# Performance work log

Hardware: AMD Instinct MI355X
Metric: run time of the kernel (lower is better)

## Reference

```python
import jax, jax.numpy as jnp
import numpy as np

B, NQ, NK, D, DV = 16, 2048, 2048, 128, 128


def setup_inputs() -> dict:
    key = jax.random.key(0)
    kq, kk, kv, kl = jax.random.split(key, 4)
    return {
        "queries": jax.random.normal(kq, (B, NQ, D), dtype=jnp.float32),
        "keys": jax.random.normal(kk, (B, NK, D), dtype=jnp.float32),
        "values": jax.random.normal(kv, (B, NK, DV), dtype=jnp.float32),
        "valid_lens": jax.random.randint(kl, (B,), 1, NK + 1, dtype=jnp.int32),
    }


def reference(queries, keys, values, valid_lens):
    d = queries.shape[-1]
    # scores: [B, NQ, NK]
    scores = jnp.einsum("bqd,bkd->bqk", queries, keys) / jnp.sqrt(jnp.float32(d))
    # mask positions >= valid_len with -1e6 (matches sequence_mask semantics)
    key_pos = jnp.arange(scores.shape[-1], dtype=jnp.int32)  # [NK]
    mask = key_pos[None, None, :] < valid_lens[:, None, None]  # [B,1,NK] -> broadcast over queries
    scores = jnp.where(mask, scores, jnp.float32(-1000000.0))
    attn = jax.nn.softmax(scores, axis=-1)
    # dropout p=0.0 -> identity
    return jnp.einsum("bqk,bkv->bqv", attn, values)
```

## Files before the change

### kernel.cpp

```cpp
#include <hip/hip_runtime.h>


#define B_   16
#define NQ_  2048
#define NK_  2048
#define D_   128
#define DV_  128
#define NTASK_ 512

typedef unsigned short ushort;
typedef __attribute__((ext_vector_type(4))) float          f32x4;
typedef __attribute__((ext_vector_type(8))) __bf16         bf16x8;
typedef __attribute__((ext_vector_type(8))) unsigned short ushort8v;
typedef __attribute__((ext_vector_type(4))) unsigned int   uint4v;

#ifdef __has_builtin
#if __has_builtin(__builtin_amdgcn_cvt_pk_bf16_f32)
#define HAVE_CVT_PK_BF16 1
#endif
#endif

__device__ __forceinline__ ushort f2bf(float f) {
    unsigned u = __builtin_bit_cast(unsigned, f);
    return (ushort)((u + 0x8000u) >> 16);
}
__device__ __forceinline__ float bf2f(ushort h) {
    unsigned u = ((unsigned)h) << 16;
    return __builtin_bit_cast(float, u);
}
__device__ __forceinline__ unsigned f2bf2(float a, float b) {
#ifdef HAVE_CVT_PK_BF16
    auto t = __builtin_amdgcn_cvt_pk_bf16_f32(a, b);
    return __builtin_bit_cast(unsigned, t);
#else
    return (unsigned)f2bf(a) | ((unsigned)f2bf(b) << 16);
#endif
}

__device__ __forceinline__ void gl_lds16(const ushort* g, ushort* l) {
    __builtin_amdgcn_global_load_lds(
        (const __attribute__((address_space(1))) void*)g,
        (__attribute__((address_space(3))) void*)l, 16, 0, 0);
}

__global__ void make_schedule(const int* __restrict__ vlen, int* __restrict__ task) {
    __shared__ int s[16];
    int tid = threadIdx.x;
    if (tid < 16) {
        int my = vlen[tid];
        int rank = 0;
        for (int o = 0; o < 16; ++o) {
            int vo = vlen[o];
            if (vo > my || (vo == my && o < tid)) ++rank;
        }
        s[rank] = tid;
    }
    __syncthreads();
    for (int e = tid; e < NTASK_; e += 64) {
        int half = e >> 8;
        int r    = e & 255;
        int p    = r >> 5;
        int qt   = r & 31;
        int b    = half ? s[15 - p] : s[p];
        task[e]  = b | (qt << 8);
    }
}

__global__ __launch_bounds__(256) void convert_kv(
    const float* __restrict__ K, const float* __restrict__ V,
    const int* __restrict__ vlen, ushort* __restrict__ Kb, ushort* __restrict__ Vtb)
{
    const int id = blockIdx.x;
    const int b  = id & 15, kt = id >> 4;
    if (kt >= ((vlen[b] + 63) >> 6)) return;
    const int tid = threadIdx.x;
    const float* gK = K + ((size_t)b * NK_ + kt * 64) * D_;
    const float* gV = V + ((size_t)b * NK_ + kt * 64) * DV_;
    ushort* tK = Kb  + ((size_t)b * 32 + kt) * 8192;
    ushort* tV = Vtb + ((size_t)b * 32 + kt) * 8192;

    #pragma unroll
    for (int i = 0; i < 4; ++i) {
        int u = i * 256 + tid;
        int key = u >> 4, d8 = u & 15;
        const float* p = gK + key * D_ + d8 * 8;
        f32x4 a0 = *(const f32x4*)p;
        f32x4 a1 = *(const f32x4*)(p + 4);
        uint4v w;
        w[0] = f2bf2(a0[0], a0[1]); w[1] = f2bf2(a0[2], a0[3]);
        w[2] = f2bf2(a1[0], a1[1]); w[3] = f2bf2(a1[2], a1[3]);
        *(uint4v*)&tK[key * 128 + ((d8 ^ (key & 7)) << 3)] = w;
    }
    #pragma unroll
    for (int i = 0; i < 4; ++i) {
        int u = i * 256 + tid;
        int dv = u & 127, kg = u >> 7;
        const float* vp = gV + (size_t)(kg * 8) * DV_ + dv;
        float v[8];
        #pragma unroll
        for (int j = 0; j < 8; ++j) v[j] = vp[(size_t)j * DV_];
        uint4v w;
        w[0] = f2bf2(v[0], v[1]); w[1] = f2bf2(v[2], v[3]);
        w[2] = f2bf2(v[4], v[5]); w[3] = f2bf2(v[6], v[7]);
        *(uint4v*)&tV[dv * 64 + ((kg ^ (dv & 7)) << 3)] = w;
    }
}

__global__ __launch_bounds__(256, 2) void attn_fwd(
    const float* __restrict__ Q, const int* __restrict__ vlen,
    const int* __restrict__ task, const ushort* __restrict__ Kb,
    const ushort* __restrict__ Vtb, float* __restrict__ Out)
{
    __shared__ ushort KVbuf[2][16384];
    __shared__ ushort Pb[4][32][40];
    __shared__ float  lsh[2][64];
    float* Osh = (float*)&KVbuf[0][0];

    const int tid  = threadIdx.x;
    const int w    = tid >> 6;
    const int wq   = w >> 1;
    const int wk   = w & 1;
    const int L    = tid & 63;
    const int col  = L & 15;
    const int quad = L >> 4;

    const int tk    = task[blockIdx.x];
    const int b     = tk & 255;
    const int qbase = (tk >> 8) * 64;
    const int vl    = vlen[b];
    const int ntiles = (vl + 63) >> 6;

    const float qscale = 0.12751743f;
    bf16x8 qf[2][4];
    #pragma unroll
    for (int q16 = 0; q16 < 2; ++q16) {
        const int qrow = qbase + wq * 32 + q16 * 16 + col;
        const float* gQ = Q + ((size_t)b * NQ_ + qrow) * D_;
        #pragma unroll
        for (int c = 0; c < 4; ++c) {
            const float* p = gQ + c * 32 + quad * 8;
            f32x4 a0 = *(const f32x4*)p;
            f32x4 a1 = *(const f32x4*)(p + 4);
            uint4v us;
            us[0] = f2bf2(a0[0] * qscale, a0[1] * qscale);
            us[1] = f2bf2(a0[2] * qscale, a0[3] * qscale);
            us[2] = f2bf2(a1[0] * qscale, a1[1] * qscale);
            us[3] = f2bf2(a1[2] * qscale, a1[3] * qscale);
            qf[q16][c] = __builtin_bit_cast(bf16x8, us);
        }
    }

    f32x4 o[2][8];
    #pragma unroll
    for (int q16 = 0; q16 < 2; ++q16)
        #pragma unroll
        for (int d = 0; d < 8; ++d) o[q16][d] = (f32x4){0.f, 0.f, 0.f, 0.f};
    float l_run[2][4] = {{0.f,0.f,0.f,0.f},{0.f,0.f,0.f,0.f}};

    const ushort* tKb = Kb  + (size_t)b * 32 * 8192;
    const ushort* tVb = Vtb + (size_t)b * 32 * 8192;

    #define ISSUE_DMA(KT, BUF)                                               \
        do {                                                                 \
            const ushort* gk = tKb + (size_t)(KT) * 8192;                    \
            const ushort* gv = tVb + (size_t)(KT) * 8192;                    \
            _Pragma("unroll")                                                \
            for (int i = 0; i < 4; ++i) {                                    \
                int off = (i * 256 + tid) * 8;                               \
                gl_lds16(gk + off, &KVbuf[BUF][off]);                        \
                gl_lds16(gv + off, &KVbuf[BUF][8192 + off]);                 \
            }                                                                \
        } while (0)

    ISSUE_DMA(0, 0);

    for (int kt = 0; kt < ntiles; ++kt) {
        const int buf = kt & 1;
        __syncthreads();
        if (kt + 1 < ntiles) ISSUE_DMA(kt + 1, buf ^ 1);

        const ushort* Kt = &KVbuf[buf][0];
        const ushort* Vt = &KVbuf[buf][8192];
        const int k0 = kt * 64;

        f32x4 s[2][2];
        #pragma unroll
        for (int kc = 0; kc < 2; ++kc) {
            const int key = wk * 32 + kc * 16 + col;
            bf16x8 kb[4];
            #pragma unroll
            for (int c = 0; c < 4; ++c)
                kb[c] = __builtin_bit_cast(bf16x8, *(const ushort8v*)
                    &Kt[key * 128 + (((c * 4 + quad) ^ (col & 7)) << 3)]);
            #pragma unroll
            for (int q16 = 0; q16 < 2; ++q16) {
                f32x4 acc = (f32x4){0.f, 0.f, 0.f, 0.f};
                #pragma unroll
                for (int c = 0; c < 4; ++c)
                    acc = __builtin_amdgcn_mfma_f32_16x16x32_bf16(qf[q16][c], kb[c], acc, 0, 0, 0);
                s[q16][kc] = acc;
            }
        }

        if (k0 + 64 > vl) {
            #pragma unroll
            for (int kc = 0; kc < 2; ++kc)
                if (k0 + wk * 32 + kc * 16 + col >= vl) {
                    s[0][kc] = (f32x4){-1e30f,-1e30f,-1e30f,-1e30f};
                    s[1][kc] = (f32x4){-1e30f,-1e30f,-1e30f,-1e30f};
                }
        }

        #pragma unroll
        for (int q16 = 0; q16 < 2; ++q16)
            #pragma unroll
            for (int kc = 0; kc < 2; ++kc)
                #pragma unroll
                for (int r = 0; r < 4; ++r) {
                    ushort pb = f2bf(exp2f(s[q16][kc][r]));
                    Pb[w][q16 * 16 + quad * 4 + r][kc * 16 + col] = pb;
                    l_run[q16][r] += bf2f(pb);
                }


        bf16x8 pa[2];
        #pragma unroll
        for (int q16 = 0; q16 < 2; ++q16)
            pa[q16] = __builtin_bit_cast(bf16x8,
                *(const ushort8v*)&Pb[w][q16 * 16 + col][quad * 8]);
        #pragma unroll
        for (int dvc = 0; dvc < 8; ++dvc) {
            const int dv = dvc * 16 + col;
            bf16x8 vb = __builtin_bit_cast(bf16x8, *(const ushort8v*)
                &Vt[dv * 64 + (((wk * 4 + quad) ^ (col & 7)) << 3)]);
            #pragma unroll
            for (int q16 = 0; q16 < 2; ++q16)
                o[q16][dvc] = __builtin_amdgcn_mfma_f32_16x16x32_bf16(pa[q16], vb, o[q16][dvc], 0, 0, 0);
        }
    }
    #undef ISSUE_DMA

    #pragma unroll
    for (int off = 1; off < 16; off <<= 1)
        #pragma unroll
        for (int q16 = 0; q16 < 2; ++q16)
            #pragma unroll
            for (int r = 0; r < 4; ++r)
                l_run[q16][r] += __shfl_xor(l_run[q16][r], off, 64);

    __syncthreads();

    if (col == 0) {
        #pragma unroll
        for (int q16 = 0; q16 < 2; ++q16)
            #pragma unroll
            for (int r = 0; r < 4; ++r)
                lsh[wk][wq * 32 + q16 * 16 + quad * 4 + r] = l_run[q16][r];
    }
    #pragma unroll
    for (int q16 = 0; q16 < 2; ++q16)
        #pragma unroll
        for (int dvc = 0; dvc < 8; ++dvc)
            #pragma unroll
            for (int r = 0; r < 4; ++r)
                Osh[wk * 8192 + (wq * 32 + q16 * 16 + quad * 4 + r) * 128 + dvc * 16 + col]
                    = o[q16][dvc][r];
    __syncthreads();

    float* gO = Out + ((size_t)b * NQ_ + qbase) * DV_;
    #pragma unroll
    for (int i = 0; i < 8; ++i) {
        int idx = i * 256 + tid;
        int row = idx >> 5;
        int dq  = idx & 31;
        f32x4 a0 = *(const f32x4*)&Osh[row * 128 + dq * 4];
        f32x4 a1 = *(const f32x4*)&Osh[8192 + row * 128 + dq * 4];
        float linv = 1.0f / (lsh[0][row] + lsh[1][row]);
        f32x4 r = (a0 + a1) * linv;
        *(f32x4*)&gO[(size_t)row * DV_ + dq * 4] = r;
    }
}

extern "C" void kernel_launch(void* const* d_in, const int* in_sizes, int n_in,
                              void* d_out, int out_size, void* d_ws, size_t ws_size,
                              hipStream_t stream) {
    const float* Q  = (const float*)d_in[0];
    const float* K  = (const float*)d_in[1];
    const float* V  = (const float*)d_in[2];
    const int*   vl = (const int*)d_in[3];
    float* out = (float*)d_out;

    char* ws = (char*)d_ws;
    int* task = (int*)ws;
    ushort* Kbuf = (ushort*)(ws + 4096);
    ushort* Vbuf = Kbuf + (size_t)B_ * 32 * 8192;

    make_schedule<<<1, 64, 0, stream>>>(vl, task);
    convert_kv<<<dim3(512, 1, 1), dim3(256, 1, 1), 0, stream>>>(K, V, vl, Kbuf, Vbuf);
    attn_fwd<<<dim3(NTASK_, 1, 1), dim3(256, 1, 1), 0, stream>>>(
        Q, vl, task, Kbuf, Vbuf, out);
}
```

Before: 138.7 us.

## Restructure attention to 8 waves per block with register P transpose

The attention kernel now uses 512 threads per block, each wave handling 16 query rows instead of 32. The score MFMA is computed transposed so that P can be rearranged in registers with permlane swaps instead of going through LDS. The scheduling kernel is folded into the attention kernel, removing one launch. The change also adds s_setprio around the MFMA sections and a cheaper row-sum reduction. This trades more waves per block and less LDS traffic for redundant per-block ranking work and a different register and occupancy profile.

```diff
diff --git a/kernel.cpp b/kernel.cpp
--- a/kernel.cpp
+++ b/kernel.cpp
@@ -23,10 +23,6 @@
 __device__ __forceinline__ ushort f2bf(float f) {
     unsigned u = __builtin_bit_cast(unsigned, f);
     return (ushort)((u + 0x8000u) >> 16);
-}
-__device__ __forceinline__ float bf2f(ushort h) {
-    unsigned u = ((unsigned)h) << 16;
-    return __builtin_bit_cast(float, u);
 }
 __device__ __forceinline__ unsigned f2bf2(float a, float b) {
 #ifdef HAVE_CVT_PK_BF16
@@ -36,34 +32,15 @@
     return (unsigned)f2bf(a) | ((unsigned)f2bf(b) << 16);
 #endif
 }
-
+__device__ __forceinline__ float bfpair_sum(unsigned u) {
+    float lo = __builtin_bit_cast(float, u << 16);
+    float hi = __builtin_bit_cast(float, u & 0xffff0000u);
+    return lo + hi;
+}
 __device__ __forceinline__ void gl_lds16(const ushort* g, ushort* l) {
     __builtin_amdgcn_global_load_lds(
         (const __attribute__((address_space(1))) void*)g,
         (__attribute__((address_space(3))) void*)l, 16, 0, 0);
-}
-
-__global__ void make_schedule(const int* __restrict__ vlen, int* __restrict__ task) {
-    __shared__ int s[16];
-    int tid = threadIdx.x;
-    if (tid < 16) {
-        int my = vlen[tid];
-        int rank = 0;
-        for (int o = 0; o < 16; ++o) {
-            int vo = vlen[o];
-            if (vo > my || (vo == my && o < tid)) ++rank;
-        }
-        s[rank] = tid;
-    }
-    __syncthreads();
-    for (int e = tid; e < NTASK_; e += 64) {
-        int half = e >> 8;
-        int r    = e & 255;
-        int p    = r >> 5;
-        int qt   = r & 31;
-        int b    = half ? s[15 - p] : s[p];
-        task[e]  = b | (qt << 8);
-    }
 }
 
 __global__ __launch_bounds__(256) void convert_kv(
@@ -106,14 +83,14 @@
     }
 }
 
-__global__ __launch_bounds__(256, 2) void attn_fwd(
+__global__ __launch_bounds__(512, 4) void attn_fwd(
     const float* __restrict__ Q, const int* __restrict__ vlen,
-    const int* __restrict__ task, const ushort* __restrict__ Kb,
-    const ushort* __restrict__ Vtb, float* __restrict__ Out)
+    const ushort* __restrict__ Kb, const ushort* __restrict__ Vtb,
+    float* __restrict__ Out)
 {
     __shared__ ushort KVbuf[2][16384];
-    __shared__ ushort Pb[4][32][40];
     __shared__ float  lsh[2][64];
+    __shared__ int    ssch[16];
     float* Osh = (float*)&KVbuf[0][0];
 
     const int tid  = threadIdx.x;
@@ -124,38 +101,47 @@
     const int col  = L & 15;
     const int quad = L >> 4;
 
-    const int tk    = task[blockIdx.x];
-    const int b     = tk & 255;
-    const int qbase = (tk >> 8) * 64;
+    if (tid < 16) {
+        int my = vlen[tid];
+        int rank = 0;
+        for (int o = 0; o < 16; ++o) {
+            int vo = vlen[o];
+            if (vo > my || (vo == my && o < tid)) ++rank;
+        }
+        ssch[rank] = tid;
+    }
+    __syncthreads();
+
+    const int e     = blockIdx.x;
+    const int p_    = (e & 255) >> 5;
+    const int b     = (e >> 8) ? ssch[15 - p_] : ssch[p_];
+    const int qbase = (e & 31) * 64;
     const int vl    = vlen[b];
     const int ntiles = (vl + 63) >> 6;
 
     const float qscale = 0.12751743f;
-    bf16x8 qf[2][4];
-    #pragma unroll
-    for (int q16 = 0; q16 < 2; ++q16) {
-        const int qrow = qbase + wq * 32 + q16 * 16 + col;
+    bf16x8 qf[4];
+    {
+        const int qrow = qbase + wq * 16 + col;
         const float* gQ = Q + ((size_t)b * NQ_ + qrow) * D_;
         #pragma unroll
         for (int c = 0; c < 4; ++c) {
-            const float* p = gQ + c * 32 + quad * 8;
-            f32x4 a0 = *(const f32x4*)p;
-            f32x4 a1 = *(const f32x4*)(p + 4);
+            const float* pp = gQ + c * 32 + quad * 8;
+            f32x4 a0 = *(const f32x4*)pp;
+            f32x4 a1 = *(const f32x4*)(pp + 4);
             uint4v us;
             us[0] = f2bf2(a0[0] * qscale, a0[1] * qscale);
             us[1] = f2bf2(a0[2] * qscale, a0[3] * qscale);
             us[2] = f2bf2(a1[0] * qscale, a1[1] * qscale);
             us[3] = f2bf2(a1[2] * qscale, a1[3] * qscale);
-            qf[q16][c] = __builtin_bit_cast(bf16x8, us);
-        }
-    }
-
-    f32x4 o[2][8];
-    #pragma unroll
-    for (int q16 = 0; q16 < 2; ++q16)
-        #pragma unroll
-        for (int d = 0; d < 8; ++d) o[q16][d] = (f32x4){0.f, 0.f, 0.f, 0.f};
-    float l_run[2][4] = {{0.f,0.f,0.f,0.f},{0.f,0.f,0.f,0.f}};
+            qf[c] = __builtin_bit_cast(bf16x8, us);
+        }
+    }
+
+    f32x4 o[8];
+    #pragma unroll
+    for (int d = 0; d < 8; ++d) o[d] = (f32x4){0.f, 0.f, 0.f, 0.f};
+    float l_run = 0.f;
 
     const ushort* tKb = Kb  + (size_t)b * 32 * 8192;
     const ushort* tVb = Vtb + (size_t)b * 32 * 8192;
@@ -165,8 +151,8 @@
             const ushort* gk = tKb + (size_t)(KT) * 8192;                    \
             const ushort* gv = tVb + (size_t)(KT) * 8192;                    \
             _Pragma("unroll")                                                \
-            for (int i = 0; i < 4; ++i) {                                    \
-                int off = (i * 256 + tid) * 8;                               \
+            for (int i = 0; i < 2; ++i) {                                    \
+                int off = (i * 512 + tid) * 8;                               \
                 gl_lds16(gk + off, &KVbuf[BUF][off]);                        \
                 gl_lds16(gv + off, &KVbuf[BUF][8192 + off]);                 \
             }                                                                \
@@ -174,6 +160,8 @@
 
     ISSUE_DMA(0, 0);
 
+    const int swz = col & 7;
+
     for (int kt = 0; kt < ntiles; ++kt) {
         const int buf = kt & 1;
         __syncthreads();
@@ -181,103 +169,86 @@
 
         const ushort* Kt = &KVbuf[buf][0];
         const ushort* Vt = &KVbuf[buf][8192];
-        const int k0 = kt * 64;
-
-        f32x4 s[2][2];
-        #pragma unroll
-        for (int kc = 0; kc < 2; ++kc) {
-            const int key = wk * 32 + kc * 16 + col;
-            bf16x8 kb[4];
+
+        f32x4 s0 = (f32x4){0.f,0.f,0.f,0.f};
+        f32x4 s1 = (f32x4){0.f,0.f,0.f,0.f};
+        __builtin_amdgcn_s_setprio(1);
+        {
+            const int key0 = (wk * 32 + col) * 128;
             #pragma unroll
-            for (int c = 0; c < 4; ++c)
-                kb[c] = __builtin_bit_cast(bf16x8, *(const ushort8v*)
-                    &Kt[key * 128 + (((c * 4 + quad) ^ (col & 7)) << 3)]);
+            for (int c = 0; c < 4; ++c) {
+                bf16x8 kb = __builtin_bit_cast(bf16x8, *(const ushort8v*)
+                    &Kt[key0 + (((c * 4 + quad) ^ swz) << 3)]);
+                s0 = __builtin_amdgcn_mfma_f32_16x16x32_bf16(kb, qf[c], s0, 0, 0, 0);
+            }
             #pragma unroll
-            for (int q16 = 0; q16 < 2; ++q16) {
-                f32x4 acc = (f32x4){0.f, 0.f, 0.f, 0.f};
-                #pragma unroll
-                for (int c = 0; c < 4; ++c)
-                    acc = __builtin_amdgcn_mfma_f32_16x16x32_bf16(qf[q16][c], kb[c], acc, 0, 0, 0);
-                s[q16][kc] = acc;
+            for (int c = 0; c < 4; ++c) {
+                bf16x8 kb = __builtin_bit_cast(bf16x8, *(const ushort8v*)
+                    &Kt[key0 + 16 * 128 + (((c * 4 + quad) ^ swz) << 3)]);
+                s1 = __builtin_amdgcn_mfma_f32_16x16x32_bf16(kb, qf[c], s1, 0, 0, 0);
             }
         }
-
-        if (k0 + 64 > vl) {
+        __builtin_amdgcn_s_setprio(0);
+
+        const int rem = vl - kt * 64 - wk * 32;
+        if (rem < 32) {
             #pragma unroll
-            for (int kc = 0; kc < 2; ++kc)
-                if (k0 + wk * 32 + kc * 16 + col >= vl) {
-                    s[0][kc] = (f32x4){-1e30f,-1e30f,-1e30f,-1e30f};
-                    s[1][kc] = (f32x4){-1e30f,-1e30f,-1e30f,-1e30f};
-                }
-        }
-
-        #pragma unroll
-        for (int q16 = 0; q16 < 2; ++q16)
-            #pragma unroll
-            for (int kc = 0; kc < 2; ++kc)
-                #pragma unroll
-                for (int r = 0; r < 4; ++r) {
-                    ushort pb = f2bf(exp2f(s[q16][kc][r]));
-                    Pb[w][q16 * 16 + quad * 4 + r][kc * 16 + col] = pb;
-                    l_run[q16][r] += bf2f(pb);
-                }
-
-
-        bf16x8 pa[2];
-        #pragma unroll
-        for (int q16 = 0; q16 < 2; ++q16)
-            pa[q16] = __builtin_bit_cast(bf16x8,
-                *(const ushort8v*)&Pb[w][q16 * 16 + col][quad * 8]);
+            for (int rr = 0; rr < 4; ++rr) {
+                if (quad * 4 + rr >= rem)      s0[rr] = -1e30f;
+                if (16 + quad * 4 + rr >= rem) s1[rr] = -1e30f;
+            }
+        }
+
+        unsigned wA = f2bf2(exp2f(s0[0]), exp2f(s0[1]));
+        unsigned wB = f2bf2(exp2f(s0[2]), exp2f(s0[3]));
+        unsigned wC = f2bf2(exp2f(s1[0]), exp2f(s1[1]));
+        unsigned wD = f2bf2(exp2f(s1[2]), exp2f(s1[3]));
+        l_run += bfpair_sum(wA) + bfpair_sum(wB) + bfpair_sum(wC) + bfpair_sum(wD);
+
+        asm("v_permlane32_swap_b32 %0, %1" : "+v"(wA), "+v"(wC));
+        asm("v_permlane32_swap_b32 %0, %1" : "+v"(wB), "+v"(wD));
+        asm("v_permlane16_swap_b32 %0, %1" : "+v"(wA), "+v"(wC));
+        asm("v_permlane16_swap_b32 %0, %1" : "+v"(wB), "+v"(wD));
+        uint4v pw;
+        pw[0] = wA; pw[1] = wB; pw[2] = wC; pw[3] = wD;
+        bf16x8 pa = __builtin_bit_cast(bf16x8, pw);
+
+        __builtin_amdgcn_s_setprio(1);
         #pragma unroll
         for (int dvc = 0; dvc < 8; ++dvc) {
             const int dv = dvc * 16 + col;
             bf16x8 vb = __builtin_bit_cast(bf16x8, *(const ushort8v*)
-                &Vt[dv * 64 + (((wk * 4 + quad) ^ (col & 7)) << 3)]);
-            #pragma unroll
-            for (int q16 = 0; q16 < 2; ++q16)
-                o[q16][dvc] = __builtin_amdgcn_mfma_f32_16x16x32_bf16(pa[q16], vb, o[q16][dvc], 0, 0, 0);
-        }
+                &Vt[dv * 64 + (((wk * 4 + quad) ^ swz) << 3)]);
+            o[dvc] = __builtin_amdgcn_mfma_f32_16x16x32_bf16(pa, vb, o[dvc], 0, 0, 0);
+        }
+        __builtin_amdgcn_s_setprio(0);
     }
     #undef ISSUE_DMA
 
-    #pragma unroll
-    for (int off = 1; off < 16; off <<= 1)
-        #pragma unroll
-        for (int q16 = 0; q16 < 2; ++q16)
-            #pragma unroll
-            for (int r = 0; r < 4; ++r)
-                l_run[q16][r] += __shfl_xor(l_run[q16][r], off, 64);
+    l_run += __shfl_xor(l_run, 16, 64);
+    l_run += __shfl_xor(l_run, 32, 64);
 
     __syncthreads();
 
-    if (col == 0) {
-        #pragma unroll
-        for (int q16 = 0; q16 < 2; ++q16)
-            #pragma unroll
-            for (int r = 0; r < 4; ++r)
-                lsh[wk][wq * 32 + q16 * 16 + quad * 4 + r] = l_run[q16][r];
-    }
-    #pragma unroll
-    for (int q16 = 0; q16 < 2; ++q16)
-        #pragma unroll
-        for (int dvc = 0; dvc < 8; ++dvc)
-            #pragma unroll
-            for (int r = 0; r < 4; ++r)
-                Osh[wk * 8192 + (wq * 32 + q16 * 16 + quad * 4 + r) * 128 + dvc * 16 + col]
-                    = o[q16][dvc][r];
+    if (L < 16) lsh[wk][wq * 16 + L] = l_run;
+    #pragma unroll
+    for (int dvc = 0; dvc < 8; ++dvc)
+        #pragma unroll
+        for (int rr = 0; rr < 4; ++rr)
+            Osh[wk * 8192 + (wq * 16 + quad * 4 + rr) * 128 + dvc * 16 + col]
+                = o[dvc][rr];
     __syncthreads();
 
     float* gO = Out + ((size_t)b * NQ_ + qbase) * DV_;
     #pragma unroll
-    for (int i = 0; i < 8; ++i) {
-        int idx = i * 256 + tid;
+    for (int i = 0; i < 4; ++i) {
+        int idx = i * 512 + tid;
         int row = idx >> 5;
         int dq  = idx & 31;
         f32x4 a0 = *(const f32x4*)&Osh[row * 128 + dq * 4];
         f32x4 a1 = *(const f32x4*)&Osh[8192 + row * 128 + dq * 4];
         float linv = 1.0f / (lsh[0][row] + lsh[1][row]);
-        f32x4 r = (a0 + a1) * linv;
-        *(f32x4*)&gO[(size_t)row * DV_ + dq * 4] = r;
+        *(f32x4*)&gO[(size_t)row * DV_ + dq * 4] = (a0 + a1) * linv;
     }
 }
 
@@ -291,12 +262,10 @@
     float* out = (float*)d_out;
 
     char* ws = (char*)d_ws;
-    int* task = (int*)ws;
     ushort* Kbuf = (ushort*)(ws + 4096);
     ushort* Vbuf = Kbuf + (size_t)B_ * 32 * 8192;
 
-    make_schedule<<<1, 64, 0, stream>>>(vl, task);
     convert_kv<<<dim3(512, 1, 1), dim3(256, 1, 1), 0, stream>>>(K, V, vl, Kbuf, Vbuf);
-    attn_fwd<<<dim3(NTASK_, 1, 1), dim3(256, 1, 1), 0, stream>>>(
-        Q, vl, task, Kbuf, Vbuf, out);
-}
+    attn_fwd<<<dim3(NTASK_, 1, 1), dim3(512, 1, 1), 0, stream>>>(
+        Q, vl, Kbuf, Vbuf, out);
+}
```

After: 132.2 us. 4.7% less time.
